# Optimization experiments

Hardware: AMD Instinct MI355X
Metric: run time of the kernel (lower is better)

The kernel has to match this reference:

```python
import jax, jax.numpy as jnp
import numpy as np

RC = 5.0                 # cutoff radius (init kwarg)
B, M = 128, 256          # structures per batch, atoms per structure
L = 17.2                 # box edge (Angstrom) -> ~0.05 atoms/A^3, ~27 nbrs/atom at rc=5
P = 2_097_152            # fixed max pair count (output padding)


def _pairs(coord):
    """Cell-list candidate generation + radius filter, batched over structures.

    Faithful to the TF CellListNL (no 'cell' / open-boundary path): atoms are
    shifted to the positive octant, binned into cells of edge rc, and candidate
    pairs are atoms of the same structure whose cell bins differ by at most 1 in
    every dimension (the 27-cell stencil). Final pairs satisfy 0 < dist < rc.
    """
    pos = coord - jnp.min(coord, axis=0)                          # [N,3] shift (as in TF code)
    cell = jnp.floor(pos / RC).astype(jnp.int32)                  # [N,3] cell bins
    posb = pos.reshape(B, M, 3)
    cellb = cell.reshape(B, M, 3)
    diff = posb[:, None, :, :] - posb[:, :, None, :]              # [B,M,M,3] = pos_j - pos_i
    sq = jnp.sum(diff * diff, axis=-1)                            # [B,M,M]
    nz = sq > 0.0
    dist = jnp.sqrt(jnp.where(nz, sq, 1.0)) * nz                  # safe norm (0 on diagonal)
    # 27-neighbor-cell stencil == per-axis bin difference in {-1,0,1}
    nbr = jnp.all(jnp.abs(cellb[:, None, :, :] - cellb[:, :, None, :]) <= 1, axis=-1)
    mask = nbr & (dist < RC) & nz                                 # [B,M,M]
    return diff, dist, mask


def setup_inputs() -> dict:
    key = jax.random.key(0)
    coord = jax.random.uniform(key, (B * M, 3), jnp.float32) * L  # atoms in [0,L)^3 per structure
    ind_1 = jnp.repeat(jnp.arange(B, dtype=jnp.int32), M)         # structure index per atom
    return {"coord": coord, "ind_1": ind_1}


def reference(coord, ind_1):
    # ind_1 is encoded structurally: atoms are laid out as B contiguous blocks of M,
    # so same-structure pairing is enforced by the batched [B,M,M] computation.
    diff, dist, mask = _pairs(coord)
    b, i, j = jnp.nonzero(mask, size=P, fill_value=0)             # fixed-size pair list
    valid = mask[b, i, j]                                         # False on padded rows
    d = dist[b, i, j] * valid                                     # [P]
    df = diff[b, i, j] * valid[:, None]                           # [P,3]
    ind_2 = jnp.stack([b * M + i, b * M + j], axis=1) * valid[:, None].astype(jnp.int32)
    return ind_2, d, df
```

## Files before the change

kernel.cpp:

```cpp
#include <hip/hip_runtime.h>
#include <float.h>

#define MM 256
#define PP 2097152
#define NBLK 512
#define CBLK 256
#define GTH (NBLK * 256)
#define CAP 2048
#define SQMAX 24.999996185302734375f

typedef unsigned long long u64;


__device__ inline void wave_min3(float& x, float& y, float& z) {
    #pragma unroll
    for (int off = 32; off > 0; off >>= 1) {
        x = fminf(x, __shfl_xor(x, off, 64));
        y = fminf(y, __shfl_xor(y, off, 64));
        z = fminf(z, __shfl_xor(z, off, 64));
    }
}

__device__ inline void flush_plane(const float* __restrict__ lds, int n, int pad,
                                   float* __restrict__ gdst, int t) {
    if (n <= 0) return;
    const int end = pad + n;
    const int nb = (end + 3) >> 2;
    for (int m = t; m < nb; m += 256) {
        const int lo = m << 2;
        if (lo >= pad && lo + 4 <= end) {
            *reinterpret_cast<float4*>(gdst + lo) =
                *reinterpret_cast<const float4*>(lds + lo);
        } else {
            const int a = lo < pad ? pad : lo;
            const int bmax = (lo + 4 < end) ? (lo + 4) : end;
            for (int e = a; e < bmax; ++e) gdst[e] = lds[e];
        }
    }
}


__global__ void __launch_bounds__(512)
count_k(const float* __restrict__ coord, float* __restrict__ minvec,
        u64* __restrict__ masks, int* __restrict__ bsums,
        float* __restrict__ outF) {
    const int cb = blockIdx.x;
    const int b = cb >> 1, h = cb & 1;
    const int t = threadIdx.x;
    const int lane = t & 63, w = t >> 6;

    __shared__ float4 tile4[4][65];
    __shared__ float lmin[3][8];
    __shared__ int wsum[8];

    {
        float4* o4 = reinterpret_cast<float4*>(outF);
        const float4 z4 = make_float4(0.f, 0.f, 0.f, 0.f);
        const int gz = cb * 512 + t;
        #pragma unroll
        for (int q = 0; q < 24; ++q) o4[gz + q * GTH] = z4;
    }

    const float4* c4 = reinterpret_cast<const float4*>(coord);
    float mx = FLT_MAX, my = FLT_MAX, mz = FLT_MAX;
    #pragma unroll 4
    for (int k = 0; k < 16; ++k) {
        const int basei = (k * 512 + t) * 3;
        const float4 f0 = c4[basei + 0];
        const float4 f1 = c4[basei + 1];
        const float4 f2 = c4[basei + 2];
        mx = fminf(mx, fminf(fminf(f0.x, f0.w), fminf(f1.z, f2.y)));
        my = fminf(my, fminf(fminf(f0.y, f1.x), fminf(f1.w, f2.z)));
        mz = fminf(mz, fminf(fminf(f0.z, f1.y), fminf(f2.x, f2.w)));
    }
    wave_min3(mx, my, mz);
    if (lane == 0) { lmin[0][w] = mx; lmin[1][w] = my; lmin[2][w] = mz; }
    __syncthreads();
    mx = fminf(fminf(fminf(lmin[0][0], lmin[0][1]), fminf(lmin[0][2], lmin[0][3])),
               fminf(fminf(lmin[0][4], lmin[0][5]), fminf(lmin[0][6], lmin[0][7])));
    my = fminf(fminf(fminf(lmin[1][0], lmin[1][1]), fminf(lmin[1][2], lmin[1][3])),
               fminf(fminf(lmin[1][4], lmin[1][5]), fminf(lmin[1][6], lmin[1][7])));
    mz = fminf(fminf(fminf(lmin[2][0], lmin[2][1]), fminf(lmin[2][2], lmin[2][3])),
               fminf(fminf(lmin[2][4], lmin[2][5]), fminf(lmin[2][6], lmin[2][7])));
    if (cb == 0 && t == 0) { minvec[0] = mx; minvec[1] = my; minvec[2] = mz; }

    if (t < 256) {
        const int ja = b * MM + t;
        tile4[t >> 6][t & 63] = make_float4(__fsub_rn(coord[3 * ja + 0], mx),
                                            __fsub_rn(coord[3 * ja + 1], my),
                                            __fsub_rn(coord[3 * ja + 2], mz), 0.0f);
    }
    __syncthreads();

    const int rblk = 2 * h + (t >> 8);
    const int tt = t & 255;
    const int i_loc = tt >> 2, c = tt & 3;
    const float4 pi4 = tile4[rblk][i_loc];
    u64 m = 0ULL;
    for (int jj = 0; jj < 64; ++jj) {
        float4 v = tile4[c][jj];
        float dx = __fsub_rn(v.x, pi4.x);
        float dy = __fsub_rn(v.y, pi4.y);
        float dz = __fsub_rn(v.z, pi4.z);
        float sq = __fadd_rn(__fadd_rn(__fmul_rn(dx, dx), __fmul_rn(dy, dy)),
                             __fmul_rn(dz, dz));
        if (sq > 0.0f && sq <= SQMAX) m |= (1ULL << jj);
    }
    masks[cb * 512 + t] = m;

    int v = __popcll(m);
    #pragma unroll
    for (int off = 32; off > 0; off >>= 1) v += __shfl_xor(v, off, 64);
    if (lane == 0) wsum[w] = v;
    __syncthreads();
    if (t == 0) {
        bsums[cb * 2 + 0] = wsum[0] + wsum[1] + wsum[2] + wsum[3];
        bsums[cb * 2 + 1] = wsum[4] + wsum[5] + wsum[6] + wsum[7];
    }
}

__global__ void __launch_bounds__(256)
write_k(const float* __restrict__ coord, const float* __restrict__ minvec,
        const u64* __restrict__ masks, const int* __restrict__ bsums,
        float* __restrict__ outF) {
    const int b2 = blockIdx.x;
    const int b = b2 >> 2, rblk = b2 & 3;
    const int t = threadIdx.x;
    const int lane = t & 63, w = t >> 6;

    __shared__ float4 tile4[4][65];
    __shared__ int pre[NBLK];
    __shared__ int wsum[4];
    __shared__ __align__(16) float sd[CAP + 4];
    __shared__ __align__(16) float sind[2 * CAP + 4];
    __shared__ __align__(16) float sdf[3 * CAP + 4];

    const float mnx = minvec[0], mny = minvec[1], mnz = minvec[2];
    const int ja = b * MM + t;
    tile4[w][lane] = make_float4(__fsub_rn(coord[3 * ja + 0], mnx),
                                 __fsub_rn(coord[3 * ja + 1], mny),
                                 __fsub_rn(coord[3 * ja + 2], mnz), 0.0f);

    if (w == 0) {
        int v[8]; int s = 0;
        #pragma unroll
        for (int q = 0; q < 8; ++q) { v[q] = bsums[lane * 8 + q]; s += v[q]; }
        int isum = s;
        #pragma unroll
        for (int off = 1; off < 64; off <<= 1) {
            int u = __shfl_up(isum, off, 64);
            if (lane >= off) isum += u;
        }
        int run = isum - s;
        #pragma unroll
        for (int q = 0; q < 8; ++q) { pre[lane * 8 + q] = run; run += v[q]; }
    }
    __syncthreads();
    const int base = pre[b2];

    const u64 mask = masks[b2 * 256 + t];
    const int cnt = __popcll(mask);
    int incl = cnt;
    #pragma unroll
    for (int off = 1; off < 64; off <<= 1) {
        int v = __shfl_up(incl, off, 64);
        if (lane >= off) incl += v;
    }
    if (lane == 63) wsum[w] = incl;
    __syncthreads();
    const int agg = wsum[0] + wsum[1] + wsum[2] + wsum[3];
    int woff = 0;
    for (int k = 0; k < w; ++k) woff += wsum[k];
    const int lexcl = woff + incl - cnt;

    const int i_loc = t >> 2, c = t & 3;
    const float4 pi4 = tile4[rblk][i_loc];
    const int gi = b * MM + rblk * 64 + i_loc;
    const int gj0 = b * MM + c * 64;

    const int nbat = (agg + CAP - 1) / CAP;
    for (int bb = 0; bb < nbat; ++bb) {
        const int wlo = bb * CAP, whi = wlo + CAP;
        const int pbase = base + wlo;
        const int pd = pbase & 3;
        const int pi = (2 * pbase) & 3;
        const int pf = (3 * pbase) & 3;
        int q = lexcl;
        u64 mm = mask;
        while (mm) {
            const int jj = __ffsll((long long)mm) - 1;
            mm &= mm - 1;
            if (q >= whi) break;
            if (q >= wlo) {
                float4 v = tile4[c][jj];
                float dx = __fsub_rn(v.x, pi4.x);
                float dy = __fsub_rn(v.y, pi4.y);
                float dz = __fsub_rn(v.z, pi4.z);
                float sq = __fadd_rn(__fadd_rn(__fmul_rn(dx, dx), __fmul_rn(dy, dy)),
                                     __fmul_rn(dz, dz));
                const int s = q - wlo;
                sd[s + pd] = __fsqrt_rn(sq);
                sind[2 * s + pi + 0] = (float)gi;
                sind[2 * s + pi + 1] = (float)(gj0 + jj);
                sdf[3 * s + pf + 0] = dx;
                sdf[3 * s + pf + 1] = dy;
                sdf[3 * s + pf + 2] = dz;
            }
            q++;
        }
        __syncthreads();
        const int nq = ((agg - wlo) < CAP) ? (agg - wlo) : CAP;
        int rem = PP - pbase; if (rem < 0) rem = 0;
        const int nv = (nq < rem) ? nq : rem;
        flush_plane(sd,   nv,     pd, outF + 2 * PP + pbase - pd,     t);
        flush_plane(sind, 2 * nv, pi, outF + 2 * pbase - pi,          t);
        flush_plane(sdf,  3 * nv, pf, outF + 3 * PP + 3 * pbase - pf, t);
        __syncthreads();
    }
}

extern "C" void kernel_launch(void* const* d_in, const int* in_sizes, int n_in,
                              void* d_out, int out_size, void* d_ws, size_t ws_size,
                              hipStream_t stream) {
    const float* coord = (const float*)d_in[0];
    float* outF = (float*)d_out;

    u64*   masks  = (u64*)d_ws;
    int*   bsums  = (int*)(masks + GTH);
    float* minvec = (float*)(bsums + NBLK);

    count_k<<<CBLK, 512, 0, stream>>>(coord, minvec, masks, bsums, outF);
    write_k<<<NBLK, 256, 0, stream>>>(coord, minvec, masks, bsums, outF);
}
```

Before: 29.52 us.

## Emit pair records in count kernel to workspace; write kernel only copies and zero-fills tail

The first kernel now compacts and writes per-block pair records (dist, indices, diff) into per-slot workspace buffers instead of just storing bitmasks. The second kernel reads the global prefix and copies each slot into the output, then zero-fills only the region past the total pair count instead of zeroing the whole output up front. This removes the recomputation and the redundant full-output zeroing that the second write used to overwrite. In exchange, every pair is written twice (workspace, then output), the workspace is much larger, and the first kernel gains serialized per-slot batches.

```diff
diff --git a/kernel.cpp b/kernel.cpp
--- a/kernel.cpp
+++ b/kernel.cpp
@@ -6,7 +6,8 @@
 #define NBLK 512
 #define CBLK 256
 #define GTH (NBLK * 256)
-#define CAP 2048
+#define CAP 1024
+#define SLOTCAP 16384
 #define SQMAX 24.999996185302734375f
 
 typedef unsigned long long u64;
@@ -21,29 +22,11 @@
     }
 }
 
-__device__ inline void flush_plane(const float* __restrict__ lds, int n, int pad,
-                                   float* __restrict__ gdst, int t) {
-    if (n <= 0) return;
-    const int end = pad + n;
-    const int nb = (end + 3) >> 2;
-    for (int m = t; m < nb; m += 256) {
-        const int lo = m << 2;
-        if (lo >= pad && lo + 4 <= end) {
-            *reinterpret_cast<float4*>(gdst + lo) =
-                *reinterpret_cast<const float4*>(lds + lo);
-        } else {
-            const int a = lo < pad ? pad : lo;
-            const int bmax = (lo + 4 < end) ? (lo + 4) : end;
-            for (int e = a; e < bmax; ++e) gdst[e] = lds[e];
-        }
-    }
-}
-
 
 __global__ void __launch_bounds__(512)
 count_k(const float* __restrict__ coord, float* __restrict__ minvec,
-        u64* __restrict__ masks, int* __restrict__ bsums,
-        float* __restrict__ outF) {
+        float* __restrict__ wsD, float* __restrict__ wsI,
+        float* __restrict__ wsF, int* __restrict__ bsums) {
     const int cb = blockIdx.x;
     const int b = cb >> 1, h = cb & 1;
     const int t = threadIdx.x;
@@ -51,15 +34,10 @@
 
     __shared__ float4 tile4[4][65];
     __shared__ float lmin[3][8];
-    __shared__ int wsum[8];
-
-    {
-        float4* o4 = reinterpret_cast<float4*>(outF);
-        const float4 z4 = make_float4(0.f, 0.f, 0.f, 0.f);
-        const int gz = cb * 512 + t;
-        #pragma unroll
-        for (int q = 0; q < 24; ++q) o4[gz + q * GTH] = z4;
-    }
+    __shared__ int wsumS[2][4];
+    __shared__ __align__(16) float sd[CAP];
+    __shared__ __align__(16) float sind[2 * CAP];
+    __shared__ __align__(16) float sdf[3 * CAP];
 
     const float4* c4 = reinterpret_cast<const float4*>(coord);
     float mx = FLT_MAX, my = FLT_MAX, mz = FLT_MAX;
@@ -92,11 +70,12 @@
     }
     __syncthreads();
 
-    const int rblk = 2 * h + (t >> 8);
+    const int sIdx = t >> 8;
+    const int rblk = 2 * h + sIdx;
     const int tt = t & 255;
     const int i_loc = tt >> 2, c = tt & 3;
     const float4 pi4 = tile4[rblk][i_loc];
-    u64 m = 0ULL;
+    u64 mask = 0ULL;
     for (int jj = 0; jj < 64; ++jj) {
         float4 v = tile4[c][jj];
         float dx = __fsub_rn(v.x, pi4.x);
@@ -104,42 +83,125 @@
         float dz = __fsub_rn(v.z, pi4.z);
         float sq = __fadd_rn(__fadd_rn(__fmul_rn(dx, dx), __fmul_rn(dy, dy)),
                              __fmul_rn(dz, dz));
-        if (sq > 0.0f && sq <= SQMAX) m |= (1ULL << jj);
-    }
-    masks[cb * 512 + t] = m;
-
-    int v = __popcll(m);
+        if (sq > 0.0f && sq <= SQMAX) mask |= (1ULL << jj);
+    }
+    const int cnt = __popcll(mask);
+    int incl = cnt;
     #pragma unroll
-    for (int off = 32; off > 0; off >>= 1) v += __shfl_xor(v, off, 64);
-    if (lane == 0) wsum[w] = v;
-    __syncthreads();
+    for (int off = 1; off < 64; off <<= 1) {
+        int v = __shfl_up(incl, off, 64);
+        if (lane >= off) incl += v;
+    }
+    if (lane == 63) wsumS[sIdx][w & 3] = incl;
+    __syncthreads();
+    const int agg0 = wsumS[0][0] + wsumS[0][1] + wsumS[0][2] + wsumS[0][3];
+    const int agg1 = wsumS[1][0] + wsumS[1][1] + wsumS[1][2] + wsumS[1][3];
+    int woff = 0;
+    for (int k = 0; k < (w & 3); ++k) woff += wsumS[sIdx][k];
+    const int lexcl = woff + incl - cnt;
     if (t == 0) {
-        bsums[cb * 2 + 0] = wsum[0] + wsum[1] + wsum[2] + wsum[3];
-        bsums[cb * 2 + 1] = wsum[4] + wsum[5] + wsum[6] + wsum[7];
+        bsums[b * 4 + 2 * h + 0] = agg0;
+        bsums[b * 4 + 2 * h + 1] = agg1;
+    }
+    __syncthreads();
+
+    const int gi = b * MM + rblk * 64 + i_loc;
+    const int gj0 = b * MM + c * 64;
+    for (int s = 0; s < 2; ++s) {
+        const int aggS = s ? agg1 : agg0;
+        const int b2 = b * 4 + 2 * h + s;
+        const int nbat = (aggS + CAP - 1) / CAP;
+        for (int bb = 0; bb < nbat; ++bb) {
+            const int wlo = bb * CAP, whi = wlo + CAP;
+            if (sIdx == s) {
+                int q = lexcl;
+                u64 mm = mask;
+                while (mm) {
+                    const int jj = __ffsll((long long)mm) - 1;
+                    mm &= mm - 1;
+                    if (q >= whi) break;
+                    if (q >= wlo) {
+                        float4 v = tile4[c][jj];
+                        float dx = __fsub_rn(v.x, pi4.x);
+                        float dy = __fsub_rn(v.y, pi4.y);
+                        float dz = __fsub_rn(v.z, pi4.z);
+                        float sq = __fadd_rn(__fadd_rn(__fmul_rn(dx, dx),
+                                                       __fmul_rn(dy, dy)),
+                                             __fmul_rn(dz, dz));
+                        const int sl = q - wlo;
+                        sd[sl] = __fsqrt_rn(sq);
+                        sind[2 * sl + 0] = (float)gi;
+                        sind[2 * sl + 1] = (float)(gj0 + jj);
+                        sdf[3 * sl + 0] = dx;
+                        sdf[3 * sl + 1] = dy;
+                        sdf[3 * sl + 2] = dz;
+                    }
+                    q++;
+                }
+            }
+            __syncthreads();
+            const int nq = ((aggS - wlo) < CAP) ? (aggS - wlo) : CAP;
+            {
+                float* dst = wsD + (size_t)b2 * SLOTCAP + wlo;
+                const int nb4 = nq >> 2;
+                for (int m = t; m < nb4; m += 512)
+                    reinterpret_cast<float4*>(dst)[m] =
+                        reinterpret_cast<const float4*>(sd)[m];
+                for (int e = (nb4 << 2) + t; e < nq; e += 512) dst[e] = sd[e];
+            }
+            {
+                float* dst = wsI + (size_t)b2 * 2 * SLOTCAP + 2 * wlo;
+                const int n2 = 2 * nq, nb4 = n2 >> 2;
+                for (int m = t; m < nb4; m += 512)
+                    reinterpret_cast<float4*>(dst)[m] =
+                        reinterpret_cast<const float4*>(sind)[m];
+                for (int e = (nb4 << 2) + t; e < n2; e += 512) dst[e] = sind[e];
+            }
+            {
+                float* dst = wsF + (size_t)b2 * 3 * SLOTCAP + 3 * wlo;
+                const int n3 = 3 * nq, nb4 = n3 >> 2;
+                for (int m = t; m < nb4; m += 512)
+                    reinterpret_cast<float4*>(dst)[m] =
+                        reinterpret_cast<const float4*>(sdf)[m];
+                for (int e = (nb4 << 2) + t; e < n3; e += 512) dst[e] = sdf[e];
+            }
+            __syncthreads();
+        }
+    }
+}
+
+__device__ inline void copy_plane(const float* __restrict__ src, int n,
+                                  float* __restrict__ dstBase, int t) {
+    if (n <= 0) return;
+    const uintptr_t addr = (uintptr_t)dstBase;
+    const int shift = (int)((addr >> 2) & 3);
+    const int nq = (n + shift + 3) >> 2;
+    float* dstQ = dstBase - shift;
+    for (int m = t; m < nq; m += 256) {
+        const int e0 = 4 * m - shift;
+        if (e0 >= 0 && e0 + 4 <= n) {
+            float4 v;
+            v.x = src[e0 + 0]; v.y = src[e0 + 1];
+            v.z = src[e0 + 2]; v.w = src[e0 + 3];
+            reinterpret_cast<float4*>(dstQ)[m] = v;
+        } else {
+            const int a = e0 < 0 ? 0 : e0;
+            const int bmax = (e0 + 4 < n) ? (e0 + 4) : n;
+            for (int e = a; e < bmax; ++e) dstBase[e] = src[e];
+        }
     }
 }
 
 __global__ void __launch_bounds__(256)
-write_k(const float* __restrict__ coord, const float* __restrict__ minvec,
-        const u64* __restrict__ masks, const int* __restrict__ bsums,
+write_k(const float* __restrict__ wsD, const float* __restrict__ wsI,
+        const float* __restrict__ wsF, const int* __restrict__ bsums,
         float* __restrict__ outF) {
     const int b2 = blockIdx.x;
-    const int b = b2 >> 2, rblk = b2 & 3;
     const int t = threadIdx.x;
     const int lane = t & 63, w = t >> 6;
 
-    __shared__ float4 tile4[4][65];
     __shared__ int pre[NBLK];
-    __shared__ int wsum[4];
-    __shared__ __align__(16) float sd[CAP + 4];
-    __shared__ __align__(16) float sind[2 * CAP + 4];
-    __shared__ __align__(16) float sdf[3 * CAP + 4];
-
-    const float mnx = minvec[0], mny = minvec[1], mnz = minvec[2];
-    const int ja = b * MM + t;
-    tile4[w][lane] = make_float4(__fsub_rn(coord[3 * ja + 0], mnx),
-                                 __fsub_rn(coord[3 * ja + 1], mny),
-                                 __fsub_rn(coord[3 * ja + 2], mnz), 0.0f);
+    __shared__ int sTot;
 
     if (w == 0) {
         int v[8]; int s = 0;
@@ -154,68 +216,41 @@
         int run = isum - s;
         #pragma unroll
         for (int q = 0; q < 8; ++q) { pre[lane * 8 + q] = run; run += v[q]; }
+        if (lane == 63) sTot = run;
     }
     __syncthreads();
     const int base = pre[b2];
-
-    const u64 mask = masks[b2 * 256 + t];
-    const int cnt = __popcll(mask);
-    int incl = cnt;
-    #pragma unroll
-    for (int off = 1; off < 64; off <<= 1) {
-        int v = __shfl_up(incl, off, 64);
-        if (lane >= off) incl += v;
-    }
-    if (lane == 63) wsum[w] = incl;
-    __syncthreads();
-    const int agg = wsum[0] + wsum[1] + wsum[2] + wsum[3];
-    int woff = 0;
-    for (int k = 0; k < w; ++k) woff += wsum[k];
-    const int lexcl = woff + incl - cnt;
-
-    const int i_loc = t >> 2, c = t & 3;
-    const float4 pi4 = tile4[rblk][i_loc];
-    const int gi = b * MM + rblk * 64 + i_loc;
-    const int gj0 = b * MM + c * 64;
-
-    const int nbat = (agg + CAP - 1) / CAP;
-    for (int bb = 0; bb < nbat; ++bb) {
-        const int wlo = bb * CAP, whi = wlo + CAP;
-        const int pbase = base + wlo;
-        const int pd = pbase & 3;
-        const int pi = (2 * pbase) & 3;
-        const int pf = (3 * pbase) & 3;
-        int q = lexcl;
-        u64 mm = mask;
-        while (mm) {
-            const int jj = __ffsll((long long)mm) - 1;
-            mm &= mm - 1;
-            if (q >= whi) break;
-            if (q >= wlo) {
-                float4 v = tile4[c][jj];
-                float dx = __fsub_rn(v.x, pi4.x);
-                float dy = __fsub_rn(v.y, pi4.y);
-                float dz = __fsub_rn(v.z, pi4.z);
-                float sq = __fadd_rn(__fadd_rn(__fmul_rn(dx, dx), __fmul_rn(dy, dy)),
-                                     __fmul_rn(dz, dz));
-                const int s = q - wlo;
-                sd[s + pd] = __fsqrt_rn(sq);
-                sind[2 * s + pi + 0] = (float)gi;
-                sind[2 * s + pi + 1] = (float)(gj0 + jj);
-                sdf[3 * s + pf + 0] = dx;
-                sdf[3 * s + pf + 1] = dy;
-                sdf[3 * s + pf + 2] = dz;
-            }
-            q++;
-        }
-        __syncthreads();
-        const int nq = ((agg - wlo) < CAP) ? (agg - wlo) : CAP;
-        int rem = PP - pbase; if (rem < 0) rem = 0;
-        const int nv = (nq < rem) ? nq : rem;
-        flush_plane(sd,   nv,     pd, outF + 2 * PP + pbase - pd,     t);
-        flush_plane(sind, 2 * nv, pi, outF + 2 * pbase - pi,          t);
-        flush_plane(sdf,  3 * nv, pf, outF + 3 * PP + 3 * pbase - pf, t);
-        __syncthreads();
+    const int aggFull = bsums[b2];
+    const int total = (sTot < PP) ? sTot : PP;
+
+    int agg = aggFull;
+    if (base >= PP) agg = 0;
+    else if (base + agg > PP) agg = PP - base;
+
+    copy_plane(wsD + (size_t)b2 * SLOTCAP,     agg,     outF + 2 * PP + base,     t);
+    copy_plane(wsI + (size_t)b2 * 2 * SLOTCAP, 2 * agg, outF + 2 * base,          t);
+    copy_plane(wsF + (size_t)b2 * 3 * SLOTCAP, 3 * agg, outF + 3 * PP + 3 * base, t);
+
+    const int g = b2 * 256 + t;
+    const float4 z4 = make_float4(0.f, 0.f, 0.f, 0.f);
+    float4* o4 = reinterpret_cast<float4*>(outF);
+    {
+        const int lo = 2 * total, hi = 2 * PP;
+        int a = (lo + 3) & ~3; if (a > hi) a = hi;
+        if (g < a - lo) outF[lo + g] = 0.0f;
+        for (int q = (a >> 2) + g; q < (hi >> 2); q += GTH) o4[q] = z4;
+    }
+    {
+        const int lo = 2 * PP + total, hi = 3 * PP;
+        int a = (lo + 3) & ~3; if (a > hi) a = hi;
+        if (g < a - lo) outF[lo + g] = 0.0f;
+        for (int q = (a >> 2) + g; q < (hi >> 2); q += GTH) o4[q] = z4;
+    }
+    {
+        const int lo = 3 * PP + 3 * total, hi = 6 * PP;
+        int a = (lo + 3) & ~3; if (a > hi) a = hi;
+        if (g < a - lo) outF[lo + g] = 0.0f;
+        for (int q = (a >> 2) + g; q < (hi >> 2); q += GTH) o4[q] = z4;
     }
 }
 
@@ -225,10 +260,12 @@
     const float* coord = (const float*)d_in[0];
     float* outF = (float*)d_out;
 
-    u64*   masks  = (u64*)d_ws;
-    int*   bsums  = (int*)(masks + GTH);
+    float* wsD    = (float*)d_ws;
+    float* wsI    = wsD + (size_t)NBLK * SLOTCAP;
+    float* wsF    = wsI + (size_t)NBLK * 2 * SLOTCAP;
+    int*   bsums  = (int*)(wsF + (size_t)NBLK * 3 * SLOTCAP);
     float* minvec = (float*)(bsums + NBLK);
 
-    count_k<<<CBLK, 512, 0, stream>>>(coord, minvec, masks, bsums, outF);
-    write_k<<<NBLK, 256, 0, stream>>>(coord, minvec, masks, bsums, outF);
-}
+    count_k<<<CBLK, 512, 0, stream>>>(coord, minvec, wsD, wsI, wsF, bsums);
+    write_k<<<NBLK, 256, 0, stream>>>(wsD, wsI, wsF, bsums, outF);
+}
```

Result: slower. 45.31 us (+53.5%).
